# Optimization experiments

Measured on AMD Instinct MI355X. Metric: run time of the kernel, lower is better.

Reference implementation:

```python
import jax, jax.numpy as jnp
import numpy as np
import math

D_MODEL = 1024
NUM_HEADS = 16
N_GROUP = 4
HEAD_DIM = D_MODEL // NUM_HEADS  # 64
KV_DIM = N_GROUP * HEAD_DIM      # 256
BS, SEQ = 2, 2048


def setup_inputs() -> dict:
    key = jax.random.key(0)
    ks = jax.random.split(key, 7)
    s = 0.02
    return {
        "h": jax.random.normal(ks[0], (BS, SEQ, D_MODEL), dtype=jnp.float32),
        "wq_w": jax.random.normal(ks[1], (D_MODEL, D_MODEL), dtype=jnp.float32) * s,
        "wq_b": jnp.zeros((D_MODEL,), dtype=jnp.float32),
        "wk_w": jax.random.normal(ks[2], (KV_DIM, D_MODEL), dtype=jnp.float32) * s,
        "wk_b": jnp.zeros((KV_DIM,), dtype=jnp.float32),
        "wv_w": jax.random.normal(ks[3], (KV_DIM, D_MODEL), dtype=jnp.float32) * s,
        "wv_b": jnp.zeros((KV_DIM,), dtype=jnp.float32),
    }


def reference(h, wq_w, wq_b, wk_w, wk_b, wv_w, wv_b):
    bs, seq, _ = h.shape
    rep = NUM_HEADS // N_GROUP  # heads per KV group

    # Linear projections (torch Linear: x @ W.T + b)
    q = h @ wq_w.T + wq_b                     # [bs, seq, d_model]
    k = h @ wk_w.T + wk_b                     # [bs, seq, kv_dim]
    v = h @ wv_w.T + wv_b                     # [bs, seq, kv_dim]

    q = q.reshape(bs, seq, NUM_HEADS, HEAD_DIM).transpose(0, 2, 1, 3)  # [b,H,s,d]
    k = k.reshape(bs, seq, N_GROUP, HEAD_DIM)                          # [b,s,G,d]
    v = v.reshape(bs, seq, N_GROUP, HEAD_DIM)
    # torch .repeat(1,1,1,rep).view(...,num_heads,head_dim) maps head h -> group h//rep,
    # identical to repeating each group `rep` times consecutively along the head axis.
    k = jnp.repeat(k, rep, axis=2).transpose(0, 2, 1, 3)               # [b,H,s,d]
    v = jnp.repeat(v, rep, axis=2).transpose(0, 2, 1, 3)               # [b,H,s,d]

    scores = jnp.einsum("bhqd,bhkd->bhqk", q, k) / math.sqrt(HEAD_DIM)
    attn = jax.nn.softmax(scores, axis=-1)
    out = jnp.einsum("bhqk,bhkd->bhqd", attn, v)                       # [b,H,s,d]
    out = out.transpose(0, 2, 1, 3).reshape(bs, seq, NUM_HEADS * HEAD_DIM)
    return out
```

## Files before the change

### kernel.cpp

```cpp
#include <hip/hip_runtime.h>

typedef _Float16 f16;
typedef _Float16 f16x8 __attribute__((ext_vector_type(8)));
typedef _Float16 f16x4 __attribute__((ext_vector_type(4)));
typedef float f32x4 __attribute__((ext_vector_type(4)));

#define MFMA16(a, b, c) __builtin_amdgcn_mfma_f32_16x16x32_f16((a), (b), (c), 0, 0, 0)

#define SEQ 2048
#define DMODEL 1024
#define NH 16
#define NG 4
#define PAD 76

__device__ __forceinline__ f16x8 cvt8(const float4 a, const float4 b) {
    f16x8 r;
    r[0] = (f16)a.x; r[1] = (f16)a.y; r[2] = (f16)a.z; r[3] = (f16)a.w;
    r[4] = (f16)b.x; r[5] = (f16)b.y; r[6] = (f16)b.z; r[7] = (f16)b.w;
    return r;
}

__global__ __launch_bounds__(256) void qkv_gemm(const float* __restrict__ hA,
                                                const float* __restrict__ wq,
                                                const float* __restrict__ wk,
                                                const float* __restrict__ wv,
                                                const float* __restrict__ bq,
                                                const float* __restrict__ bk,
                                                const float* __restrict__ bv,
                                                f16* __restrict__ Qb,
                                                f16* __restrict__ Kb,
                                                f16* __restrict__ Vtb,
                                                float qscale) {
    __shared__ __align__(16) f16 As[128 * 32];
    __shared__ __align__(16) f16 Bs[128 * 32];

    const int tid  = threadIdx.x;
    const int lane = tid & 63;
    const int l15  = lane & 15;
    const int l4   = lane >> 4;
    const int wave = tid >> 6;
    const int wm   = (wave >> 1) * 64;
    const int wn   = (wave & 1) * 64;
    const int bx   = blockIdx.x;
    const int m0   = blockIdx.y * 128;

    const float* W; const float* bias; f16* C; int N, n0; float osc; int vmode;
    if (bx < 8)       { W = wq; bias = bq; C = Qb;  N = 1024; n0 = bx * 128;        osc = qscale; vmode = 0; }
    else if (bx < 10) { W = wk; bias = bk; C = Kb;  N = 256;  n0 = (bx - 8) * 128;  osc = 1.0f;   vmode = 0; }
    else              { W = wv; bias = bv; C = Vtb; N = 256;  n0 = (bx - 10) * 128; osc = 1.0f;   vmode = 1; }

    const int rowT = tid >> 2;
    const int colT = (tid & 3) * 8;
    const float* Ag = hA + (size_t)(m0 + rowT) * DMODEL + colT;
    const float* Bg = W  + (size_t)(n0 + rowT) * DMODEL + colT;

    f32x4 acc[4][4];
#pragma unroll
    for (int i = 0; i < 4; i++)
#pragma unroll
        for (int j = 0; j < 4; j++) acc[i][j] = (f32x4)0.0f;

    float4 ra[4], rb[4];
    ra[0] = *(const float4*)(Ag);
    ra[1] = *(const float4*)(Ag + 4);
    ra[2] = *(const float4*)(Ag + (size_t)64 * DMODEL);
    ra[3] = *(const float4*)(Ag + (size_t)64 * DMODEL + 4);
    rb[0] = *(const float4*)(Bg);
    rb[1] = *(const float4*)(Bg + 4);
    rb[2] = *(const float4*)(Bg + (size_t)64 * DMODEL);
    rb[3] = *(const float4*)(Bg + (size_t)64 * DMODEL + 4);

    for (int k0 = 0; k0 < DMODEL; k0 += 32) {
        __syncthreads();
        *(f16x8*)&As[rowT * 32 + colT]        = cvt8(ra[0], ra[1]);
        *(f16x8*)&As[(rowT + 64) * 32 + colT] = cvt8(ra[2], ra[3]);
        *(f16x8*)&Bs[rowT * 32 + colT]        = cvt8(rb[0], rb[1]);
        *(f16x8*)&Bs[(rowT + 64) * 32 + colT] = cvt8(rb[2], rb[3]);
        if (k0 + 32 < DMODEL) {
            const int kn = k0 + 32;
            ra[0] = *(const float4*)(Ag + kn);
            ra[1] = *(const float4*)(Ag + kn + 4);
            ra[2] = *(const float4*)(Ag + (size_t)64 * DMODEL + kn);
            ra[3] = *(const float4*)(Ag + (size_t)64 * DMODEL + kn + 4);
            rb[0] = *(const float4*)(Bg + kn);
            rb[1] = *(const float4*)(Bg + kn + 4);
            rb[2] = *(const float4*)(Bg + (size_t)64 * DMODEL + kn);
            rb[3] = *(const float4*)(Bg + (size_t)64 * DMODEL + kn + 4);
        }
        __syncthreads();

        f16x8 af[4], bf[4];
#pragma unroll
        for (int i = 0; i < 4; i++)
            af[i] = *(const f16x8*)&As[(wm + i * 16 + l15) * 32 + l4 * 8];
#pragma unroll
        for (int j = 0; j < 4; j++)
            bf[j] = *(const f16x8*)&Bs[(wn + j * 16 + l15) * 32 + l4 * 8];
#pragma unroll
        for (int i = 0; i < 4; i++)
#pragma unroll
            for (int j = 0; j < 4; j++)
                acc[i][j] = MFMA16(af[i], bf[j], acc[i][j]);
    }

#pragma unroll
    for (int i = 0; i < 4; i++) {
        const int mbase = m0 + wm + i * 16 + l4 * 4;
#pragma unroll
        for (int j = 0; j < 4; j++) {
            const int n  = n0 + wn + j * 16 + l15;
            const float bv = bias[n];
            if (vmode == 0) {
#pragma unroll
                for (int r = 0; r < 4; r++)
                    C[(size_t)(mbase + r) * N + n] = (f16)((acc[i][j][r] + bv) * osc);
            } else {
                f16x4 p;
#pragma unroll
                for (int r = 0; r < 4; r++)
                    p[r] = (f16)((acc[i][j][r] + bv) * osc);
                const int bb = mbase >> 11;
                const int s  = mbase & 2047;
                *(f16x4*)&C[((size_t)(bb * 256 + n)) * SEQ + s] = p;
            }
        }
    }
}

__global__ __launch_bounds__(256, 4) void attn_kernel(const f16* __restrict__ Q,
                                                      const f16* __restrict__ Kt,
                                                      const f16* __restrict__ Vt,
                                                      float* __restrict__ out) {
    __shared__ __align__(16) f16 Ks[64 * PAD];
    __shared__ __align__(16) f16 Vs[64 * PAD];
    __shared__ __align__(16) f16 Ps[64 * PAD];

    const int tid  = threadIdx.x;
    const int lane = tid & 63;
    const int l15  = lane & 15;
    const int l4   = lane >> 4;
    const int wave = tid >> 6;
    const int b    = blockIdx.z;
    const int hh   = blockIdx.y;
    const int g    = hh >> 2;
    const int q0   = blockIdx.x * 64;
    const int qw   = wave * 16;

    f16x8 qf[2];
#pragma unroll
    for (int kt = 0; kt < 2; kt++)
        qf[kt] = *(const f16x8*)&Q[((size_t)(b * SEQ + q0 + qw + l15)) * DMODEL + hh * 64 + kt * 32 + l4 * 8];

    f32x4 oacc[4];
    float lsum[4];
#pragma unroll
    for (int dt = 0; dt < 4; dt++) oacc[dt] = (f32x4)0.0f;
#pragma unroll
    for (int r = 0; r < 4; r++) lsum[r] = 0.0f;

    const int srow = tid >> 2;
    const int sc8  = (tid & 3) * 8;
    const f16* Kg = Kt + (size_t)(b * SEQ + srow) * 256 + g * 64 + sc8;
    const f16* Vg = Vt + (size_t)(b * 256 + g * 64 + srow) * SEQ + sc8;

    for (int kb = 0; kb < SEQ; kb += 64) {
        *(f16x8*)&Ks[srow * PAD + sc8]      = *(const f16x8*)(Kg + (size_t)kb * 256);
        *(f16x8*)&Ks[srow * PAD + 32 + sc8] = *(const f16x8*)(Kg + (size_t)kb * 256 + 32);
        *(f16x8*)&Vs[srow * PAD + sc8]      = *(const f16x8*)(Vg + kb);
        *(f16x8*)&Vs[srow * PAD + 32 + sc8] = *(const f16x8*)(Vg + kb + 32);
        __syncthreads();

        f32x4 sacc[4];
#pragma unroll
        for (int jt = 0; jt < 4; jt++) sacc[jt] = (f32x4)0.0f;
#pragma unroll
        for (int jt = 0; jt < 4; jt++) {
            const f16x8 kf0 = *(const f16x8*)&Ks[(jt * 16 + l15) * PAD + l4 * 8];
            const f16x8 kf1 = *(const f16x8*)&Ks[(jt * 16 + l15) * PAD + 32 + l4 * 8];
            sacc[jt] = MFMA16(qf[0], kf0, sacc[jt]);
            sacc[jt] = MFMA16(qf[1], kf1, sacc[jt]);
        }

#pragma unroll
        for (int jt = 0; jt < 4; jt++)
#pragma unroll
            for (int r = 0; r < 4; r++) {
                const float p = exp2f(fminf(sacc[jt][r], 14.0f));
                lsum[r] += p;
                Ps[(qw + l4 * 4 + r) * PAD + jt * 16 + l15] = (f16)p;
            }

#pragma unroll
        for (int kt = 0; kt < 2; kt++) {
            const f16x8 pf = *(const f16x8*)&Ps[(qw + l15) * PAD + kt * 32 + l4 * 8];
#pragma unroll
            for (int dt = 0; dt < 4; dt++) {
                const f16x8 vf = *(const f16x8*)&Vs[(dt * 16 + l15) * PAD + kt * 32 + l4 * 8];
                oacc[dt] = MFMA16(pf, vf, oacc[dt]);
            }
        }
        __syncthreads();
    }

#pragma unroll
    for (int r = 0; r < 4; r++) {
        float l = lsum[r];
        l += __shfl_xor(l, 1);
        l += __shfl_xor(l, 2);
        l += __shfl_xor(l, 4);
        l += __shfl_xor(l, 8);
        const float inv = 1.0f / l;
        const int q = q0 + qw + l4 * 4 + r;
        float* op = out + ((size_t)(b * SEQ + q)) * DMODEL + hh * 64;
#pragma unroll
        for (int dt = 0; dt < 4; dt++)
            op[dt * 16 + l15] = oacc[dt][r] * inv;
    }
}

extern "C" void kernel_launch(void* const* d_in, const int* in_sizes, int n_in,
                              void* d_out, int out_size, void* d_ws, size_t ws_size,
                              hipStream_t stream) {
    const float* h    = (const float*)d_in[0];
    const float* wq_w = (const float*)d_in[1];
    const float* wq_b = (const float*)d_in[2];
    const float* wk_w = (const float*)d_in[3];
    const float* wk_b = (const float*)d_in[4];
    const float* wv_w = (const float*)d_in[5];
    const float* wv_b = (const float*)d_in[6];
    float* out = (float*)d_out;

    char* ws = (char*)d_ws;
    f16* Qb  = (f16*)(ws + 0);
    f16* Kb  = (f16*)(ws + 8388608);
    f16* Vtb = (f16*)(ws + 10485760);

    const float qscale = 0.125f * 1.4426950408889634f;
    qkv_gemm<<<dim3(12, 32), 256, 0, stream>>>(h, wq_w, wk_w, wv_w, wq_b, wk_b, wv_b,
                                               Qb, Kb, Vtb, qscale);

    attn_kernel<<<dim3(32, 16, 2), 256, 0, stream>>>(Qb, Kb, Vtb, out);
}
```

Baseline: 187.5 us.

## Load K/V fragments directly into registers and double query rows per wave

The attention kernel no longer stages K and V through shared memory. Each wave loads its MFMA fragments straight from global memory into registers, prefetching the next K tile during the PV step, which removes both __syncthreads per iteration. Each wave now handles 32 query rows instead of 16, so the block covers 128 queries and the grid is halved, and the MFMA sections are wrapped in s_setprio. In exchange, every wave issues its own redundant K/V global loads (relying on cache), register pressure rises, and the fewer blocks may lower occupancy.

```diff
diff --git a/kernel.cpp b/kernel.cpp
--- a/kernel.cpp
+++ b/kernel.cpp
@@ -127,13 +127,11 @@
     }
 }
 
-__global__ __launch_bounds__(256, 4) void attn_kernel(const f16* __restrict__ Q,
-                                                      const f16* __restrict__ Kt,
-                                                      const f16* __restrict__ Vt,
-                                                      float* __restrict__ out) {
-    __shared__ __align__(16) f16 Ks[64 * PAD];
-    __shared__ __align__(16) f16 Vs[64 * PAD];
-    __shared__ __align__(16) f16 Ps[64 * PAD];
+__global__ __launch_bounds__(256) void attn_kernel(const f16* __restrict__ Q,
+                                                   const f16* __restrict__ Kt,
+                                                   const f16* __restrict__ Vt,
+                                                   float* __restrict__ out) {
+    __shared__ __align__(16) f16 Ps[128 * PAD];
 
     const int tid  = threadIdx.x;
     const int lane = tid & 63;
@@ -143,79 +141,113 @@
     const int b    = blockIdx.z;
     const int hh   = blockIdx.y;
     const int g    = hh >> 2;
-    const int q0   = blockIdx.x * 64;
-    const int qw   = wave * 16;
-
-    f16x8 qf[2];
-#pragma unroll
-    for (int kt = 0; kt < 2; kt++)
-        qf[kt] = *(const f16x8*)&Q[((size_t)(b * SEQ + q0 + qw + l15)) * DMODEL + hh * 64 + kt * 32 + l4 * 8];
-
-    f32x4 oacc[4];
-    float lsum[4];
-#pragma unroll
-    for (int dt = 0; dt < 4; dt++) oacc[dt] = (f32x4)0.0f;
-#pragma unroll
-    for (int r = 0; r < 4; r++) lsum[r] = 0.0f;
-
-    const int srow = tid >> 2;
-    const int sc8  = (tid & 3) * 8;
-    const f16* Kg = Kt + (size_t)(b * SEQ + srow) * 256 + g * 64 + sc8;
-    const f16* Vg = Vt + (size_t)(b * 256 + g * 64 + srow) * SEQ + sc8;
+    const int q0   = blockIdx.x * 128;
+    const int qw   = wave * 32;
+
+    f16x8 qf[2][2];
+#pragma unroll
+    for (int rg = 0; rg < 2; rg++)
+#pragma unroll
+        for (int kt = 0; kt < 2; kt++)
+            qf[rg][kt] = *(const f16x8*)&Q[((size_t)(b * SEQ + q0 + qw + rg * 16 + l15)) * DMODEL
+                                           + hh * 64 + kt * 32 + l4 * 8];
+
+    f32x4 oacc[2][4];
+    float lsum[2][4];
+#pragma unroll
+    for (int rg = 0; rg < 2; rg++) {
+#pragma unroll
+        for (int dt = 0; dt < 4; dt++) oacc[rg][dt] = (f32x4)0.0f;
+#pragma unroll
+        for (int r = 0; r < 4; r++) lsum[rg][r] = 0.0f;
+    }
+
+    const f16* Kg = Kt + ((size_t)(b * SEQ) + l15) * 256 + g * 64 + l4 * 8;
+    const f16* Vg = Vt + ((size_t)(b * 256 + g * 64 + l15)) * SEQ + l4 * 8;
+
+    f16x8 kf[2][4], vf[2][4];
+#pragma unroll
+    for (int jt = 0; jt < 4; jt++)
+#pragma unroll
+        for (int kt = 0; kt < 2; kt++)
+            kf[kt][jt] = *(const f16x8*)(Kg + (size_t)(jt * 16) * 256 + kt * 32);
 
     for (int kb = 0; kb < SEQ; kb += 64) {
-        *(f16x8*)&Ks[srow * PAD + sc8]      = *(const f16x8*)(Kg + (size_t)kb * 256);
-        *(f16x8*)&Ks[srow * PAD + 32 + sc8] = *(const f16x8*)(Kg + (size_t)kb * 256 + 32);
-        *(f16x8*)&Vs[srow * PAD + sc8]      = *(const f16x8*)(Vg + kb);
-        *(f16x8*)&Vs[srow * PAD + 32 + sc8] = *(const f16x8*)(Vg + kb + 32);
-        __syncthreads();
-
-        f32x4 sacc[4];
-#pragma unroll
-        for (int jt = 0; jt < 4; jt++) sacc[jt] = (f32x4)0.0f;
-#pragma unroll
-        for (int jt = 0; jt < 4; jt++) {
-            const f16x8 kf0 = *(const f16x8*)&Ks[(jt * 16 + l15) * PAD + l4 * 8];
-            const f16x8 kf1 = *(const f16x8*)&Ks[(jt * 16 + l15) * PAD + 32 + l4 * 8];
-            sacc[jt] = MFMA16(qf[0], kf0, sacc[jt]);
-            sacc[jt] = MFMA16(qf[1], kf1, sacc[jt]);
-        }
-
+        f32x4 sacc[2][4];
+#pragma unroll
+        for (int rg = 0; rg < 2; rg++)
+#pragma unroll
+            for (int jt = 0; jt < 4; jt++) sacc[rg][jt] = (f32x4)0.0f;
+
+        __builtin_amdgcn_s_setprio(1);
 #pragma unroll
         for (int jt = 0; jt < 4; jt++)
 #pragma unroll
-            for (int r = 0; r < 4; r++) {
-                const float p = exp2f(fminf(sacc[jt][r], 14.0f));
-                lsum[r] += p;
-                Ps[(qw + l4 * 4 + r) * PAD + jt * 16 + l15] = (f16)p;
+            for (int rg = 0; rg < 2; rg++) {
+                sacc[rg][jt] = MFMA16(qf[rg][0], kf[0][jt], sacc[rg][jt]);
+                sacc[rg][jt] = MFMA16(qf[rg][1], kf[1][jt], sacc[rg][jt]);
             }
-
-#pragma unroll
-        for (int kt = 0; kt < 2; kt++) {
-            const f16x8 pf = *(const f16x8*)&Ps[(qw + l15) * PAD + kt * 32 + l4 * 8];
-#pragma unroll
-            for (int dt = 0; dt < 4; dt++) {
-                const f16x8 vf = *(const f16x8*)&Vs[(dt * 16 + l15) * PAD + kt * 32 + l4 * 8];
-                oacc[dt] = MFMA16(pf, vf, oacc[dt]);
-            }
-        }
-        __syncthreads();
-    }
-
-#pragma unroll
-    for (int r = 0; r < 4; r++) {
-        float l = lsum[r];
-        l += __shfl_xor(l, 1);
-        l += __shfl_xor(l, 2);
-        l += __shfl_xor(l, 4);
-        l += __shfl_xor(l, 8);
-        const float inv = 1.0f / l;
-        const int q = q0 + qw + l4 * 4 + r;
-        float* op = out + ((size_t)(b * SEQ + q)) * DMODEL + hh * 64;
+        __builtin_amdgcn_s_setprio(0);
+
 #pragma unroll
         for (int dt = 0; dt < 4; dt++)
-            op[dt * 16 + l15] = oacc[dt][r] * inv;
-    }
+#pragma unroll
+            for (int kt = 0; kt < 2; kt++)
+                vf[kt][dt] = *(const f16x8*)(Vg + (size_t)(dt * 16) * SEQ + kb + kt * 32);
+
+#pragma unroll
+        for (int rg = 0; rg < 2; rg++)
+#pragma unroll
+            for (int jt = 0; jt < 4; jt++)
+#pragma unroll
+                for (int r = 0; r < 4; r++) {
+                    const float p = exp2f(fminf(sacc[rg][jt][r], 14.0f));
+                    lsum[rg][r] += p;
+                    Ps[(qw + rg * 16 + l4 * 4 + r) * PAD + jt * 16 + l15] = (f16)p;
+                }
+
+        f16x8 pf[2][2];
+#pragma unroll
+        for (int rg = 0; rg < 2; rg++)
+#pragma unroll
+            for (int kt = 0; kt < 2; kt++)
+                pf[rg][kt] = *(const f16x8*)&Ps[(qw + rg * 16 + l15) * PAD + kt * 32 + l4 * 8];
+
+        if (kb + 64 < SEQ) {
+#pragma unroll
+            for (int jt = 0; jt < 4; jt++)
+#pragma unroll
+                for (int kt = 0; kt < 2; kt++)
+                    kf[kt][jt] = *(const f16x8*)(Kg + (size_t)(kb + 64 + jt * 16) * 256 + kt * 32);
+        }
+
+        __builtin_amdgcn_s_setprio(1);
+#pragma unroll
+        for (int kt = 0; kt < 2; kt++)
+#pragma unroll
+            for (int rg = 0; rg < 2; rg++)
+#pragma unroll
+                for (int dt = 0; dt < 4; dt++)
+                    oacc[rg][dt] = MFMA16(pf[rg][kt], vf[kt][dt], oacc[rg][dt]);
+        __builtin_amdgcn_s_setprio(0);
+    }
+
+#pragma unroll
+    for (int rg = 0; rg < 2; rg++)
+#pragma unroll
+        for (int r = 0; r < 4; r++) {
+            float l = lsum[rg][r];
+            l += __shfl_xor(l, 1);
+            l += __shfl_xor(l, 2);
+            l += __shfl_xor(l, 4);
+            l += __shfl_xor(l, 8);
+            const float inv = 1.0f / l;
+            const int q = q0 + qw + rg * 16 + l4 * 4 + r;
+            float* op = out + ((size_t)(b * SEQ + q)) * DMODEL + hh * 64;
+#pragma unroll
+            for (int dt = 0; dt < 4; dt++)
+                op[dt * 16 + l15] = oacc[rg][dt][r] * inv;
+        }
 }
 
 extern "C" void kernel_launch(void* const* d_in, const int* in_sizes, int n_in,
@@ -239,5 +271,5 @@
     qkv_gemm<<<dim3(12, 32), 256, 0, stream>>>(h, wq_w, wk_w, wv_w, wq_b, wk_b, wv_b,
                                                Qb, Kb, Vtb, qscale);
 
-    attn_kernel<<<dim3(32, 16, 2), 256, 0, stream>>>(Qb, Kb, Vtb, out);
-}
+    attn_kernel<<<dim3(16, 16, 2), 256, 0, stream>>>(Qb, Kb, Vtb, out);
+}
```

Result: slower. 223.6 us (+19.3%).

## Pre-convert inputs to fp16 and use direct global-to-LDS double-buffered GEMM loads

Applied to the files above, without the earlier changes.

Adds a separate kernel that converts h and the three weight matrices to fp16 in workspace. The QKV GEMM then streams fp16 tiles straight into LDS with global_load_lds into a double buffer, which drops register staging and in-loop conversion and halves the bytes per tile. It also raises wave priority around the MFMA block. The cost is an extra kernel launch plus a full read and write pass over h and the weights, and the double-buffer synchronisation relies on a single barrier per iteration.

```diff
diff --git a/kernel.cpp b/kernel.cpp
--- a/kernel.cpp
+++ b/kernel.cpp
@@ -20,19 +20,54 @@
     return r;
 }
 
-__global__ __launch_bounds__(256) void qkv_gemm(const float* __restrict__ hA,
-                                                const float* __restrict__ wq,
-                                                const float* __restrict__ wk,
-                                                const float* __restrict__ wv,
-                                                const float* __restrict__ bq,
-                                                const float* __restrict__ bk,
-                                                const float* __restrict__ bv,
-                                                f16* __restrict__ Qb,
-                                                f16* __restrict__ Kb,
-                                                f16* __restrict__ Vtb,
-                                                float qscale) {
-    __shared__ __align__(16) f16 As[128 * 32];
-    __shared__ __align__(16) f16 Bs[128 * 32];
+__device__ __forceinline__ void gl_lds16(f16* lds, const f16* g) {
+    __builtin_amdgcn_global_load_lds(
+        (const __attribute__((address_space(1))) void*)g,
+        (__attribute__((address_space(3))) void*)lds, 16, 0, 0);
+}
+
+#define HN  (4096 * 1024)
+#define WQN (1024 * 1024)
+#define WKN (256 * 1024)
+#define WVN (256 * 1024)
+#define TOT8 ((HN + WQN + WKN + WVN) / 8)
+
+__global__ __launch_bounds__(256) void cvt_kernel(const float* __restrict__ h,
+                                                  const float* __restrict__ wq,
+                                                  const float* __restrict__ wk,
+                                                  const float* __restrict__ wv,
+                                                  f16* __restrict__ h16,
+                                                  f16* __restrict__ W16) {
+    const int c = blockIdx.x * 256 + threadIdx.x;
+    if (c >= TOT8) return;
+    const size_t e = (size_t)c * 8;
+    const float* src;
+    f16* dst;
+    if (e < HN) {
+        src = h + e; dst = h16 + e;
+    } else {
+        const size_t e2 = e - HN;
+        if (e2 < WQN)            src = wq + e2;
+        else if (e2 < WQN + WKN) src = wk + (e2 - WQN);
+        else                     src = wv + (e2 - WQN - WKN);
+        dst = W16 + e2;
+    }
+    const float4 a = *(const float4*)src;
+    const float4 b = *(const float4*)(src + 4);
+    *(f16x8*)dst = cvt8(a, b);
+}
+
+__global__ __launch_bounds__(256) void qkv_gemm16(const f16* __restrict__ A,
+                                                  const f16* __restrict__ W,
+                                                  const float* __restrict__ bq,
+                                                  const float* __restrict__ bk,
+                                                  const float* __restrict__ bv,
+                                                  f16* __restrict__ Qb,
+                                                  f16* __restrict__ Kb,
+                                                  f16* __restrict__ Vtb,
+                                                  float qscale) {
+    __shared__ __align__(16) f16 As[2][128 * 32];
+    __shared__ __align__(16) f16 Bs[2][128 * 32];
 
     const int tid  = threadIdx.x;
     const int lane = tid & 63;
@@ -43,16 +78,11 @@
     const int wn   = (wave & 1) * 64;
     const int bx   = blockIdx.x;
     const int m0   = blockIdx.y * 128;
-
-    const float* W; const float* bias; f16* C; int N, n0; float osc; int vmode;
-    if (bx < 8)       { W = wq; bias = bq; C = Qb;  N = 1024; n0 = bx * 128;        osc = qscale; vmode = 0; }
-    else if (bx < 10) { W = wk; bias = bk; C = Kb;  N = 256;  n0 = (bx - 8) * 128;  osc = 1.0f;   vmode = 0; }
-    else              { W = wv; bias = bv; C = Vtb; N = 256;  n0 = (bx - 10) * 128; osc = 1.0f;   vmode = 1; }
-
-    const int rowT = tid >> 2;
-    const int colT = (tid & 3) * 8;
-    const float* Ag = hA + (size_t)(m0 + rowT) * DMODEL + colT;
-    const float* Bg = W  + (size_t)(n0 + rowT) * DMODEL + colT;
+    const int n0g  = bx * 128;
+
+    const f16* Ag = A + ((size_t)(m0 + (lane >> 2))) * 1024 + (lane & 3) * 8;
+    const f16* Wg = W + ((size_t)(n0g + (lane >> 2))) * 1024 + (lane & 3) * 8;
+    const size_t rstep = (size_t)16 * 1024;
 
     f32x4 acc[4][4];
 #pragma unroll
@@ -60,48 +90,52 @@
 #pragma unroll
         for (int j = 0; j < 4; j++) acc[i][j] = (f32x4)0.0f;
 
-    float4 ra[4], rb[4];
-    ra[0] = *(const float4*)(Ag);
-    ra[1] = *(const float4*)(Ag + 4);
-    ra[2] = *(const float4*)(Ag + (size_t)64 * DMODEL);
-    ra[3] = *(const float4*)(Ag + (size_t)64 * DMODEL + 4);
-    rb[0] = *(const float4*)(Bg);
-    rb[1] = *(const float4*)(Bg + 4);
-    rb[2] = *(const float4*)(Bg + (size_t)64 * DMODEL);
-    rb[3] = *(const float4*)(Bg + (size_t)64 * DMODEL + 4);
-
+    {
+        f16* Ad = &As[0][(wave * 2) * 512];
+        f16* Bd = &Bs[0][(wave * 2) * 512];
+        gl_lds16(Ad,       Ag + (size_t)(wave * 2) * rstep);
+        gl_lds16(Ad + 512, Ag + (size_t)(wave * 2 + 1) * rstep);
+        gl_lds16(Bd,       Wg + (size_t)(wave * 2) * rstep);
+        gl_lds16(Bd + 512, Wg + (size_t)(wave * 2 + 1) * rstep);
+    }
+
+    int cur = 0;
     for (int k0 = 0; k0 < DMODEL; k0 += 32) {
         __syncthreads();
-        *(f16x8*)&As[rowT * 32 + colT]        = cvt8(ra[0], ra[1]);
-        *(f16x8*)&As[(rowT + 64) * 32 + colT] = cvt8(ra[2], ra[3]);
-        *(f16x8*)&Bs[rowT * 32 + colT]        = cvt8(rb[0], rb[1]);
-        *(f16x8*)&Bs[(rowT + 64) * 32 + colT] = cvt8(rb[2], rb[3]);
         if (k0 + 32 < DMODEL) {
+            const int nxt = cur ^ 1;
+            f16* Ad = &As[nxt][(wave * 2) * 512];
+            f16* Bd = &Bs[nxt][(wave * 2) * 512];
             const int kn = k0 + 32;
-            ra[0] = *(const float4*)(Ag + kn);
-            ra[1] = *(const float4*)(Ag + kn + 4);
-            ra[2] = *(const float4*)(Ag + (size_t)64 * DMODEL + kn);
-            ra[3] = *(const float4*)(Ag + (size_t)64 * DMODEL + kn + 4);
-            rb[0] = *(const float4*)(Bg + kn);
-            rb[1] = *(const float4*)(Bg + kn + 4);
-            rb[2] = *(const float4*)(Bg + (size_t)64 * DMODEL + kn);
-            rb[3] = *(const float4*)(Bg + (size_t)64 * DMODEL + kn + 4);
-        }
-        __syncthreads();
-
+            gl_lds16(Ad,       Ag + (size_t)(wave * 2) * rstep + kn);
+            gl_lds16(Ad + 512, Ag + (size_t)(wave * 2 + 1) * rstep + kn);
+            gl_lds16(Bd,       Wg + (size_t)(wave * 2) * rstep + kn);
+            gl_lds16(Bd + 512, Wg + (size_t)(wave * 2 + 1) * rstep + kn);
+        }
+
+        const f16* Ab = As[cur];
+        const f16* Bb = Bs[cur];
         f16x8 af[4], bf[4];
 #pragma unroll
         for (int i = 0; i < 4; i++)
-            af[i] = *(const f16x8*)&As[(wm + i * 16 + l15) * 32 + l4 * 8];
+            af[i] = *(const f16x8*)&Ab[(wm + i * 16 + l15) * 32 + l4 * 8];
 #pragma unroll
         for (int j = 0; j < 4; j++)
-            bf[j] = *(const f16x8*)&Bs[(wn + j * 16 + l15) * 32 + l4 * 8];
+            bf[j] = *(const f16x8*)&Bb[(wn + j * 16 + l15) * 32 + l4 * 8];
+        __builtin_amdgcn_s_setprio(1);
 #pragma unroll
         for (int i = 0; i < 4; i++)
 #pragma unroll
             for (int j = 0; j < 4; j++)
                 acc[i][j] = MFMA16(af[i], bf[j], acc[i][j]);
-    }
+        __builtin_amdgcn_s_setprio(0);
+        cur ^= 1;
+    }
+
+    const float* bias; f16* C; int N, n0; float osc; int vmode;
+    if (bx < 8)       { bias = bq; C = Qb;  N = 1024; n0 = bx * 128;        osc = qscale; vmode = 0; }
+    else if (bx < 10) { bias = bk; C = Kb;  N = 256;  n0 = (bx - 8) * 128;  osc = 1.0f;   vmode = 0; }
+    else              { bias = bv; C = Vtb; N = 256;  n0 = (bx - 10) * 128; osc = 1.0f;   vmode = 1; }
 
 #pragma unroll
     for (int i = 0; i < 4; i++) {
@@ -109,19 +143,19 @@
 #pragma unroll
         for (int j = 0; j < 4; j++) {
             const int n  = n0 + wn + j * 16 + l15;
-            const float bv = bias[n];
+            const float bb = bias[n];
             if (vmode == 0) {
 #pragma unroll
                 for (int r = 0; r < 4; r++)
-                    C[(size_t)(mbase + r) * N + n] = (f16)((acc[i][j][r] + bv) * osc);
+                    C[(size_t)(mbase + r) * N + n] = (f16)((acc[i][j][r] + bb) * osc);
             } else {
                 f16x4 p;
 #pragma unroll
                 for (int r = 0; r < 4; r++)
-                    p[r] = (f16)((acc[i][j][r] + bv) * osc);
-                const int bb = mbase >> 11;
-                const int s  = mbase & 2047;
-                *(f16x4*)&C[((size_t)(bb * 256 + n)) * SEQ + s] = p;
+                    p[r] = (f16)((acc[i][j][r] + bb) * osc);
+                const int batch = mbase >> 11;
+                const int s     = mbase & 2047;
+                *(f16x4*)&C[((size_t)(batch * 256 + n)) * SEQ + s] = p;
             }
         }
     }
@@ -234,10 +268,13 @@
     f16* Qb  = (f16*)(ws + 0);
     f16* Kb  = (f16*)(ws + 8388608);
     f16* Vtb = (f16*)(ws + 10485760);
+    f16* h16 = (f16*)(ws + 12582912);
+    f16* W16 = (f16*)(ws + 20971520);
 
     const float qscale = 0.125f * 1.4426950408889634f;
-    qkv_gemm<<<dim3(12, 32), 256, 0, stream>>>(h, wq_w, wk_w, wv_w, wq_b, wk_b, wv_b,
-                                               Qb, Kb, Vtb, qscale);
-
+
+    cvt_kernel<<<dim3(TOT8 / 256), 256, 0, stream>>>(h, wq_w, wk_w, wv_w, h16, W16);
+    qkv_gemm16<<<dim3(12, 32), 256, 0, stream>>>(h16, W16, wq_b, wk_b, wv_b,
+                                                 Qb, Kb, Vtb, qscale);
     attn_kernel<<<dim3(32, 16, 2), 256, 0, stream>>>(Qb, Kb, Vtb, out);
 }
```

Result: no change. 188.5 us (+0.5%).
